# Optimization experiments

Hardware: AMD Instinct MI355X
Metric: run time of the kernel (lower is better)

## Reference

```python
import jax, jax.numpy as jnp
import numpy as np

T, N, C, D, K = 512, 256, 128, 128, 128

def setup_inputs() -> dict:
    key = jax.random.key(0)
    ks = jax.random.split(key, 6)
    s = 1.0 / np.sqrt(D)
    return {
        "x":   jax.random.normal(ks[0], (T, N, C), dtype=jnp.float32),
        "W_x": jax.random.normal(ks[1], (D, C), dtype=jnp.float32) * s,  # torch Linear: (out,in)
        "b_x": jax.random.normal(ks[2], (D,), dtype=jnp.float32) * s,
        "W_h": jax.random.normal(ks[3], (D, D), dtype=jnp.float32) * s,
        "W_y": jax.random.normal(ks[4], (K, D), dtype=jnp.float32) * s,
        "b_y": jax.random.normal(ks[5], (K,), dtype=jnp.float32) * s,
    }

def reference(x, W_x, b_x, W_h, W_y, b_y):
    # Elman RNN: h_t = relu(x_t @ W_x^T + b_x + h_{t-1} @ W_h^T)
    # Precompute the input projection for all timesteps in one big GEMM,
    # then scan only the true recurrent dependency.
    xproj = jnp.einsum('tnc,dc->tnd', x, W_x) + b_x  # (T, N, D)

    def step(h, xp_t):
        h_new = jax.nn.relu(xp_t + h @ W_h.T)  # (N, D)
        return h_new, h_new

    h0 = jnp.zeros((x.shape[1], W_h.shape[0]), dtype=x.dtype)
    _, all_h = jax.lax.scan(step, h0, xproj)          # (T, N, D)
    all_y = jnp.einsum('tnd,kd->tnk', all_h, W_y) + b_y  # (T, N, K)
    return all_y, all_h
```

## Files before the change

### kernel.cpp

```cpp
#include <hip/hip_runtime.h>

static constexpr int T_STEPS = 512;
static constexpr int NBATCH  = 256;
static constexpr int DD      = 128;
static constexpr long TND    = (long)T_STEPS * NBATCH * DD;

typedef short bf16x8 __attribute__((ext_vector_type(8)));
typedef float f32x4  __attribute__((ext_vector_type(4)));

__device__ inline unsigned short f2bf(float f) {
  unsigned u = __builtin_bit_cast(unsigned, f);
  unsigned r = u + 0x7FFFu + ((u >> 16) & 1u);
  return (unsigned short)(r >> 16);
}

__device__ inline bf16x8 pack8(const float* s) {
  bf16x8 v;
#pragma unroll
  for (int i = 0; i < 8; ++i) v[i] = (short)f2bf(s[i]);
  return v;
}

__global__ __launch_bounds__(256) void gemm128_mfma(
    const float* __restrict__ A, const float* __restrict__ W,
    const float* __restrict__ bias, float* __restrict__ O, int ntiles) {
  const int lane = threadIdx.x & 63;
  const int wib  = threadIdx.x >> 6;
  const int m    = lane & 15;
  const int q    = lane >> 4;

  bf16x8 Wf[8][4];
#pragma unroll
  for (int j = 0; j < 8; ++j)
#pragma unroll
    for (int kq = 0; kq < 4; ++kq) {
      const float* p = W + (j * 16 + m) * DD + kq * 32 + q * 8;
      float t[8];
      *(float4*)&t[0] = *(const float4*)p;
      *(float4*)&t[4] = *(const float4*)(p + 4);
      Wf[j][kq] = pack8(t);
    }
  float bv[8];
#pragma unroll
  for (int j = 0; j < 8; ++j) bv[j] = bias[j * 16 + m];

  const int wglobal = blockIdx.x * 4 + wib;
  const int nwaves  = gridDim.x * 4;
  for (int tile = wglobal; tile < ntiles; tile += nwaves) {
    const long r0 = (long)tile * 16;
    f32x4 acc[8];
#pragma unroll
    for (int j = 0; j < 8; ++j) acc[j] = (f32x4){0.f, 0.f, 0.f, 0.f};

#pragma unroll
    for (int kq = 0; kq < 4; ++kq) {
      const float* p = A + (r0 + m) * DD + kq * 32 + q * 8;
      float t[8];
      *(float4*)&t[0] = *(const float4*)p;
      *(float4*)&t[4] = *(const float4*)(p + 4);
      bf16x8 af = pack8(t);
#pragma unroll
      for (int j = 0; j < 8; ++j)
        acc[j] = __builtin_amdgcn_mfma_f32_16x16x32_bf16(af, Wf[j][kq], acc[j], 0, 0, 0);
    }
#pragma unroll
    for (int j = 0; j < 8; ++j)
#pragma unroll
      for (int r = 0; r < 4; ++r)
        O[(r0 + q * 4 + r) * DD + j * 16 + m] = acc[j][r] + bv[j];
  }
}

__global__ __launch_bounds__(128) void rnn_scan(
    const float* __restrict__ Wh, float* __restrict__ H ) {
  const int tid = threadIdx.x;
  const int jc  = tid & 3;
  const int c   = tid >> 2;
  const int n   = blockIdx.x;

  float w[4][32];
#pragma unroll
  for (int s = 0; s < 4; ++s)
#pragma unroll
    for (int qq = 0; qq < 8; ++qq) {
      float4 wv = *(const float4*)(Wh + (4 * c + s) * DD + jc * 32 + qq * 4);
      w[s][qq * 4 + 0] = wv.x; w[s][qq * 4 + 1] = wv.y;
      w[s][qq * 4 + 2] = wv.z; w[s][qq * 4 + 3] = wv.w;
    }

  __shared__ __align__(16) float hb[2][144];
  for (int i = tid; i < 2 * 144; i += 128) (&hb[0][0])[i] = 0.f;

  const long step = (long)NBATCH * DD;
  float* base = H + (long)n * DD + 4 * c;

  float4 xpb[8], xpn[8];
#pragma unroll
  for (int i = 0; i < 8; ++i) xpb[i] = *(const float4*)(base + (long)i * step);
  __syncthreads();

  int p = 0;
#pragma unroll 1
  for (int ch = 0; ch < 64; ++ch) {
    const long tn0 = (ch < 63) ? (long)(ch + 1) * 8 : 63L * 8;
#pragma unroll
    for (int i = 0; i < 8; ++i) xpn[i] = *(const float4*)(base + (tn0 + i) * step);

    float4 hsv[8];
#pragma unroll
    for (int ti = 0; ti < 8; ++ti) {
      float a0 = 0.f, a1 = 0.f, a2 = 0.f, a3 = 0.f;
#pragma unroll
      for (int qq = 0; qq < 8; ++qq) {
        float4 h4 = *(const float4*)&hb[p][jc * 36 + qq * 4];
        a0 += h4.x * w[0][qq*4] + h4.y * w[0][qq*4+1] + h4.z * w[0][qq*4+2] + h4.w * w[0][qq*4+3];
        a1 += h4.x * w[1][qq*4] + h4.y * w[1][qq*4+1] + h4.z * w[1][qq*4+2] + h4.w * w[1][qq*4+3];
        a2 += h4.x * w[2][qq*4] + h4.y * w[2][qq*4+1] + h4.z * w[2][qq*4+2] + h4.w * w[2][qq*4+3];
        a3 += h4.x * w[3][qq*4] + h4.y * w[3][qq*4+1] + h4.z * w[3][qq*4+2] + h4.w * w[3][qq*4+3];
      }
      a0 += __shfl_xor(a0, 1); a0 += __shfl_xor(a0, 2);
      a1 += __shfl_xor(a1, 1); a1 += __shfl_xor(a1, 2);
      a2 += __shfl_xor(a2, 1); a2 += __shfl_xor(a2, 2);
      a3 += __shfl_xor(a3, 1); a3 += __shfl_xor(a3, 2);

      if (jc == 0) {
        float4 hv;
        hv.x = fmaxf(a0 + xpb[ti].x, 0.f);
        hv.y = fmaxf(a1 + xpb[ti].y, 0.f);
        hv.z = fmaxf(a2 + xpb[ti].z, 0.f);
        hv.w = fmaxf(a3 + xpb[ti].w, 0.f);
        const int pos = 4 * c + 4 * (c >> 3);
        *(float4*)&hb[p ^ 1][pos] = hv;
        hsv[ti] = hv;
      }
      __syncthreads();
      p ^= 1;
    }

    if (jc == 0) {
#pragma unroll
      for (int ti = 0; ti < 8; ++ti)
        *(float4*)(base + (long)(ch * 8 + ti) * step) = hsv[ti];
    }
#pragma unroll
    for (int i = 0; i < 8; ++i) xpb[i] = xpn[i];
  }
}

extern "C" void kernel_launch(void* const* d_in, const int* in_sizes, int n_in,
                              void* d_out, int out_size, void* d_ws, size_t ws_size,
                              hipStream_t stream) {
  const float* x  = (const float*)d_in[0];
  const float* Wx = (const float*)d_in[1];
  const float* bx = (const float*)d_in[2];
  const float* Wh = (const float*)d_in[3];
  const float* Wy = (const float*)d_in[4];
  const float* by = (const float*)d_in[5];

  float* Y = (float*)d_out;
  float* H = (float*)d_out + TND;

  const int ntiles = T_STEPS * NBATCH / 16;

  gemm128_mfma<<<512, 256, 0, stream>>>(x, Wx, bx, H, ntiles);
  rnn_scan<<<NBATCH, 128, 0, stream>>>(Wh, H);
  gemm128_mfma<<<512, 256, 0, stream>>>(H, Wy, by, Y, ntiles);
}
```

Baseline: 561.4 us.

## Widen RNN scan to 256 threads and prefetch A tiles in GEMM

The recurrent scan now uses 256 threads per batch row. Each group of 16 lanes covers 8 output dims with an 8-wide dot-product slice, and a 16-lane butterfly shuffle reduces the partial sums. This shortens the per-step serial dot-product chain at the cost of more shuffles and a select for the writer lane. The GEMM kernel software-prefetches the next tile's A rows into registers, uses the library bf16x2 packed conversion, declares 2 blocks per CU in launch bounds, and launches twice as many blocks. Register pressure may rise from the prefetch buffers.

```diff
diff --git a/kernel.cpp b/kernel.cpp
--- a/kernel.cpp
+++ b/kernel.cpp
@@ -1,4 +1,5 @@
 #include <hip/hip_runtime.h>
+#include <hip/hip_bf16.h>
 
 static constexpr int T_STEPS = 512;
 static constexpr int NBATCH  = 256;
@@ -8,20 +9,23 @@
 typedef short bf16x8 __attribute__((ext_vector_type(8)));
 typedef float f32x4  __attribute__((ext_vector_type(4)));
 
-__device__ inline unsigned short f2bf(float f) {
-  unsigned u = __builtin_bit_cast(unsigned, f);
-  unsigned r = u + 0x7FFFu + ((u >> 16) & 1u);
-  return (unsigned short)(r >> 16);
+__device__ inline void pk2(short* dst, float a, float b) {
+  __hip_bfloat162 h = __float22bfloat162_rn(make_float2(a, b));
+  short2 s;
+  __builtin_memcpy(&s, &h, sizeof(s));
+  dst[0] = s.x; dst[1] = s.y;
 }
-
-__device__ inline bf16x8 pack8(const float* s) {
+__device__ inline bf16x8 pack8(float4 a, float4 b) {
+  short t[8];
+  pk2(t + 0, a.x, a.y); pk2(t + 2, a.z, a.w);
+  pk2(t + 4, b.x, b.y); pk2(t + 6, b.z, b.w);
   bf16x8 v;
 #pragma unroll
-  for (int i = 0; i < 8; ++i) v[i] = (short)f2bf(s[i]);
+  for (int i = 0; i < 8; ++i) v[i] = t[i];
   return v;
 }
 
-__global__ __launch_bounds__(256) void gemm128_mfma(
+__global__ __launch_bounds__(256, 2) void gemm128_mfma(
     const float* __restrict__ A, const float* __restrict__ W,
     const float* __restrict__ bias, float* __restrict__ O, int ntiles) {
   const int lane = threadIdx.x & 63;
@@ -35,115 +39,140 @@
 #pragma unroll
     for (int kq = 0; kq < 4; ++kq) {
       const float* p = W + (j * 16 + m) * DD + kq * 32 + q * 8;
-      float t[8];
-      *(float4*)&t[0] = *(const float4*)p;
-      *(float4*)&t[4] = *(const float4*)(p + 4);
-      Wf[j][kq] = pack8(t);
+      Wf[j][kq] = pack8(*(const float4*)p, *(const float4*)(p + 4));
     }
   float bv[8];
 #pragma unroll
   for (int j = 0; j < 8; ++j) bv[j] = bias[j * 16 + m];
 
-  const int wglobal = blockIdx.x * 4 + wib;
-  const int nwaves  = gridDim.x * 4;
-  for (int tile = wglobal; tile < ntiles; tile += nwaves) {
-    const long r0 = (long)tile * 16;
+  int tile = blockIdx.x * 4 + wib;
+  const int nw = gridDim.x * 4;
+  if (tile >= ntiles) return;
+
+  float4 cur[8];
+  {
+    const float* ap = A + ((long)tile * 16 + m) * DD + q * 8;
+#pragma unroll
+    for (int kq = 0; kq < 4; ++kq) {
+      cur[2 * kq]     = *(const float4*)(ap + kq * 32);
+      cur[2 * kq + 1] = *(const float4*)(ap + kq * 32 + 4);
+    }
+  }
+
+  for (;;) {
+    const int nt   = tile + nw;
+    const bool more = nt < ntiles;
+    float4 nxt[8];
+    if (more) {
+      const float* np = A + ((long)nt * 16 + m) * DD + q * 8;
+#pragma unroll
+      for (int kq = 0; kq < 4; ++kq) {
+        nxt[2 * kq]     = *(const float4*)(np + kq * 32);
+        nxt[2 * kq + 1] = *(const float4*)(np + kq * 32 + 4);
+      }
+    }
+
     f32x4 acc[8];
 #pragma unroll
     for (int j = 0; j < 8; ++j) acc[j] = (f32x4){0.f, 0.f, 0.f, 0.f};
-
 #pragma unroll
     for (int kq = 0; kq < 4; ++kq) {
-      const float* p = A + (r0 + m) * DD + kq * 32 + q * 8;
-      float t[8];
-      *(float4*)&t[0] = *(const float4*)p;
-      *(float4*)&t[4] = *(const float4*)(p + 4);
-      bf16x8 af = pack8(t);
+      bf16x8 af = pack8(cur[2 * kq], cur[2 * kq + 1]);
 #pragma unroll
       for (int j = 0; j < 8; ++j)
         acc[j] = __builtin_amdgcn_mfma_f32_16x16x32_bf16(af, Wf[j][kq], acc[j], 0, 0, 0);
     }
+
+    const long r0 = (long)tile * 16;
 #pragma unroll
     for (int j = 0; j < 8; ++j)
 #pragma unroll
       for (int r = 0; r < 4; ++r)
         O[(r0 + q * 4 + r) * DD + j * 16 + m] = acc[j][r] + bv[j];
+
+    if (!more) break;
+#pragma unroll
+    for (int i = 0; i < 8; ++i) cur[i] = nxt[i];
+    tile = nt;
   }
 }
 
-__global__ __launch_bounds__(128) void rnn_scan(
+__global__ __launch_bounds__(256) void rnn_scan(
     const float* __restrict__ Wh, float* __restrict__ H ) {
   const int tid = threadIdx.x;
-  const int jc  = tid & 3;
-  const int c   = tid >> 2;
+  const int g   = tid & 15;
+  const int c   = tid >> 4;
   const int n   = blockIdx.x;
 
-  float w[4][32];
+  float w[8][8];
 #pragma unroll
-  for (int s = 0; s < 4; ++s)
-#pragma unroll
-    for (int qq = 0; qq < 8; ++qq) {
-      float4 wv = *(const float4*)(Wh + (4 * c + s) * DD + jc * 32 + qq * 4);
-      w[s][qq * 4 + 0] = wv.x; w[s][qq * 4 + 1] = wv.y;
-      w[s][qq * 4 + 2] = wv.z; w[s][qq * 4 + 3] = wv.w;
-    }
+  for (int s = 0; s < 8; ++s) {
+    const float* p = Wh + (c * 8 + s) * DD + g * 8;
+    float4 w0 = *(const float4*)p, w1 = *(const float4*)(p + 4);
+    w[s][0] = w0.x; w[s][1] = w0.y; w[s][2] = w0.z; w[s][3] = w0.w;
+    w[s][4] = w1.x; w[s][5] = w1.y; w[s][6] = w1.z; w[s][7] = w1.w;
+  }
 
   __shared__ __align__(16) float hb[2][144];
-  for (int i = tid; i < 2 * 144; i += 128) (&hb[0][0])[i] = 0.f;
+  for (int i = tid; i < 2 * 144; i += 256) (&hb[0][0])[i] = 0.f;
 
   const long step = (long)NBATCH * DD;
-  float* base = H + (long)n * DD + 4 * c;
+  const bool wr  = (g < 8);
+  const int  d   = c * 8 + g;
+  const int  dpos = d + 4 * (d >> 5);
+  float* gp = H + (long)n * DD + d;
 
-  float4 xpb[8], xpn[8];
+  float xpc[8], xpn[8], hs[8];
+  if (wr) {
 #pragma unroll
-  for (int i = 0; i < 8; ++i) xpb[i] = *(const float4*)(base + (long)i * step);
+    for (int i = 0; i < 8; ++i) xpc[i] = gp[(long)i * step];
+  }
   __syncthreads();
 
+  const int jadd = g * 8 + 4 * (g >> 2);
   int p = 0;
 #pragma unroll 1
   for (int ch = 0; ch < 64; ++ch) {
     const long tn0 = (ch < 63) ? (long)(ch + 1) * 8 : 63L * 8;
+    if (wr) {
 #pragma unroll
-    for (int i = 0; i < 8; ++i) xpn[i] = *(const float4*)(base + (tn0 + i) * step);
+      for (int i = 0; i < 8; ++i) xpn[i] = gp[(tn0 + i) * step];
+    }
 
-    float4 hsv[8];
 #pragma unroll
     for (int ti = 0; ti < 8; ++ti) {
-      float a0 = 0.f, a1 = 0.f, a2 = 0.f, a3 = 0.f;
+      float4 h0 = *(const float4*)&hb[p][jadd];
+      float4 h1 = *(const float4*)&hb[p][jadd + 4];
+      float a[8];
 #pragma unroll
-      for (int qq = 0; qq < 8; ++qq) {
-        float4 h4 = *(const float4*)&hb[p][jc * 36 + qq * 4];
-        a0 += h4.x * w[0][qq*4] + h4.y * w[0][qq*4+1] + h4.z * w[0][qq*4+2] + h4.w * w[0][qq*4+3];
-        a1 += h4.x * w[1][qq*4] + h4.y * w[1][qq*4+1] + h4.z * w[1][qq*4+2] + h4.w * w[1][qq*4+3];
-        a2 += h4.x * w[2][qq*4] + h4.y * w[2][qq*4+1] + h4.z * w[2][qq*4+2] + h4.w * w[2][qq*4+3];
-        a3 += h4.x * w[3][qq*4] + h4.y * w[3][qq*4+1] + h4.z * w[3][qq*4+2] + h4.w * w[3][qq*4+3];
+      for (int s = 0; s < 8; ++s)
+        a[s] = h0.x * w[s][0] + h0.y * w[s][1] + h0.z * w[s][2] + h0.w * w[s][3]
+             + h1.x * w[s][4] + h1.y * w[s][5] + h1.z * w[s][6] + h1.w * w[s][7];
+#pragma unroll
+      for (int s = 0; s < 8; ++s) {
+        a[s] += __shfl_xor(a[s], 1);
+        a[s] += __shfl_xor(a[s], 2);
+        a[s] += __shfl_xor(a[s], 4);
+        a[s] += __shfl_xor(a[s], 8);
       }
-      a0 += __shfl_xor(a0, 1); a0 += __shfl_xor(a0, 2);
-      a1 += __shfl_xor(a1, 1); a1 += __shfl_xor(a1, 2);
-      a2 += __shfl_xor(a2, 1); a2 += __shfl_xor(a2, 2);
-      a3 += __shfl_xor(a3, 1); a3 += __shfl_xor(a3, 2);
-
-      if (jc == 0) {
-        float4 hv;
-        hv.x = fmaxf(a0 + xpb[ti].x, 0.f);
-        hv.y = fmaxf(a1 + xpb[ti].y, 0.f);
-        hv.z = fmaxf(a2 + xpb[ti].z, 0.f);
-        hv.w = fmaxf(a3 + xpb[ti].w, 0.f);
-        const int pos = 4 * c + 4 * (c >> 3);
-        *(float4*)&hb[p ^ 1][pos] = hv;
-        hsv[ti] = hv;
+      if (wr) {
+        float sel = a[0];
+#pragma unroll
+        for (int s = 1; s < 8; ++s) sel = (g == s) ? a[s] : sel;
+        float hv = fmaxf(sel + xpc[ti], 0.f);
+        hb[p ^ 1][dpos] = hv;
+        hs[ti] = hv;
       }
       __syncthreads();
       p ^= 1;
     }
 
-    if (jc == 0) {
+    if (wr) {
 #pragma unroll
-      for (int ti = 0; ti < 8; ++ti)
-        *(float4*)(base + (long)(ch * 8 + ti) * step) = hsv[ti];
+      for (int i = 0; i < 8; ++i) gp[(long)(ch * 8 + i) * step] = hs[i];
     }
 #pragma unroll
-    for (int i = 0; i < 8; ++i) xpb[i] = xpn[i];
+    for (int i = 0; i < 8; ++i) xpc[i] = xpn[i];
   }
 }
 
@@ -162,7 +191,7 @@
 
   const int ntiles = T_STEPS * NBATCH / 16;
 
-  gemm128_mfma<<<512, 256, 0, stream>>>(x, Wx, bx, H, ntiles);
-  rnn_scan<<<NBATCH, 128, 0, stream>>>(Wh, H);
-  gemm128_mfma<<<512, 256, 0, stream>>>(H, Wy, by, Y, ntiles);
+  gemm128_mfma<<<1024, 256, 0, stream>>>(x, Wx, bx, H, ntiles);
+  rnn_scan<<<NBATCH, 256, 0, stream>>>(Wh, H);
+  gemm128_mfma<<<1024, 256, 0, stream>>>(H, Wy, by, Y, ntiles);
 }
```

After: 590.8 us. 5.2% more time.
